# Performance work log

Measured on AMD Instinct MI355X. Metric: run time of the kernel, lower is better.

Reference implementation:

```python
import jax, jax.numpy as jnp
import numpy as np

B, S, E, H, FFN, NQ = 4, 2048, 1024, 16, 4096, 8
DK = E // H
EPS = 1e-5


def setup_inputs() -> dict:
    key = jax.random.key(0)
    ks = jax.random.split(key, 8)
    x = jax.random.normal(ks[0], (B, S, E), dtype=jnp.float32)
    theta = jax.random.normal(ks[1], (NQ,), dtype=jnp.float32)  # RY angles
    w1 = jax.random.normal(ks[2], (FFN, NQ), dtype=jnp.float32) / np.sqrt(NQ)
    b1 = jnp.zeros((FFN,), dtype=jnp.float32)
    w2 = jax.random.normal(ks[3], (E, FFN), dtype=jnp.float32) / np.sqrt(FFN)
    b2 = jnp.zeros((E,), dtype=jnp.float32)
    gamma1 = jnp.ones((E,), dtype=jnp.float32)
    beta1 = jnp.zeros((E,), dtype=jnp.float32)
    gamma2 = jnp.ones((E,), dtype=jnp.float32)
    beta2 = jnp.zeros((E,), dtype=jnp.float32)
    return {"x": x, "theta": theta, "w1": w1, "b1": b1, "w2": w2, "b2": b2,
            "gamma1": gamma1, "beta1": beta1, "gamma2": gamma2, "beta2": beta2}


def _layernorm(h, g, b):
    mu = jnp.mean(h, axis=-1, keepdims=True)
    var = jnp.mean(jnp.square(h - mu), axis=-1, keepdims=True)
    return (h - mu) * jax.lax.rsqrt(var + EPS) * g + b


def _attention(x):
    # q = k = v = separate_heads(x); no projection weights in the original.
    q = x.reshape(B, S, H, DK).transpose(0, 2, 1, 3)  # [B,H,S,DK]
    scores = jnp.einsum("bhqd,bhkd->bhqk", q, q) / np.sqrt(DK)
    probs = jax.nn.softmax(scores, axis=-1)
    out = jnp.einsum("bhqk,bhkd->bhqd", probs, q)
    return out.transpose(0, 2, 1, 3).reshape(B, S, E)


def _ffn_quantum(h, theta, w1, b1, w2, b2):
    # Per-token circuit: RX(x_i) then RY(theta_i) on independent qubits,
    # measure PauliZ -> <Z_i> = cos(x_i) * cos(theta_i). Batched over all tokens.
    qout = jnp.cos(h[..., :NQ]) * jnp.cos(theta)  # [B,S,NQ]
    hid = jax.nn.relu(jnp.einsum("bsq,fq->bsf", qout, w1) + b1)
    return jnp.einsum("bsf,ef->bse", hid, w2) + b2


def reference(x, theta, w1, b1, w2, b2, gamma1, beta1, gamma2, beta2):
    attn_out = _attention(x)
    h = _layernorm(x + attn_out, gamma1, beta1)
    ffn_out = _ffn_quantum(h, theta, w1, b1, w2, b2)
    return _layernorm(h + ffn_out, gamma2, beta2)
```

## Files before the change

kernel.cpp:

```cpp
#include <hip/hip_runtime.h>


#define Bq 4
#define Sq 2048
#define Eq 1024
#define Hq 16
#define DKq 64
#define FFNq 4096
#define NQq 8
#define LOG2E 1.44269504f

typedef unsigned int u32;
typedef unsigned short u16;
typedef _Float16 f16;
typedef f16 f16x8 __attribute__((ext_vector_type(8)));
typedef __fp16 fp16x2 __attribute__((ext_vector_type(2)));
typedef float f32x4 __attribute__((ext_vector_type(4)));
typedef float f32x16 __attribute__((ext_vector_type(16)));
typedef u32 u32x2 __attribute__((ext_vector_type(2)));
typedef u32 u32x4 __attribute__((ext_vector_type(4)));

#if __has_builtin(__builtin_amdgcn_exp2f)
#define EXP2F __builtin_amdgcn_exp2f
#else
#define EXP2F exp2f
#endif

#define MFMA(a, b, c) __builtin_amdgcn_mfma_f32_16x16x32_f16((a), (b), (c), 0, 0, 0)
#define MFMA32(a, b, c) __builtin_amdgcn_mfma_f32_32x32x16_f16((a), (b), (c), 0, 0, 0)

#define GLL(g, l)                                                          \
  __builtin_amdgcn_global_load_lds(                                        \
      (const __attribute__((address_space(1))) u32*)(g),                   \
      (__attribute__((address_space(3))) u32*)(l), 16, 0, 0)

__device__ __forceinline__ u16 f2h(float x) {
  f16 t = (f16)x;
  return __builtin_bit_cast(u16, t);
}
__device__ __forceinline__ float h2f(u16 w) {
  return (float)__builtin_bit_cast(f16, w);
}
#if __has_builtin(__builtin_amdgcn_cvt_pkrtz)
__device__ __forceinline__ u32 pkrtz(float a, float b) {
  fp16x2 r = __builtin_amdgcn_cvt_pkrtz(a, b);
  return __builtin_bit_cast(u32, r);
}
#else
__device__ __forceinline__ u32 pkrtz(float a, float b) {
  return (u32)f2h(a) | ((u32)f2h(b) << 16);
}
#endif

__device__ __forceinline__ void swap32(u32 a, u32 b, u32& r0, u32& r1) {
#if __has_builtin(__builtin_amdgcn_permlane32_swap)
  u32x2 r = __builtin_amdgcn_permlane32_swap(a, b, false, false);
  r0 = r[0];
  r1 = r[1];
#else
  u32 ax = (u32)__shfl_xor((int)a, 32);
  u32 bx = (u32)__shfl_xor((int)b, 32);
  const bool lo = (threadIdx.x & 32) == 0;
  r0 = lo ? a : bx;
  r1 = lo ? ax : b;
#endif
}

union F8 { f16x8 v; u32 w[4]; u16 h[8]; f16 e[8]; };

__global__ void k_cvt(const float* __restrict__ src, uint4* __restrict__ dst, int n8) {
  int i = blockIdx.x * 256 + threadIdx.x;
  if (i >= n8) return;
  const float4* s = (const float4*)src + 2 * (long)i;
  float4 a = s[0], b = s[1];
  uint4 r;
  r.x = pkrtz(a.x, a.y);
  r.y = pkrtz(a.z, a.w);
  r.z = pkrtz(b.x, b.y);
  r.w = pkrtz(b.z, b.w);
  dst[i] = r;
}

__global__ void k_prep(const float* __restrict__ x, u16* __restrict__ xh,
                       u16* __restrict__ xt) {
  __shared__ u16 tile[64 * 72];
  const int tid = threadIdx.x;
  const int bx = blockIdx.x;
  const int sb = bx & 31, bh = bx >> 5;
  const int b = bh >> 4, h = bh & 15;
  const int s0 = sb * 64;
  const int r = tid >> 2, cq = tid & 3;
  const float* xp = x + ((long)(b * Sq + s0 + r)) * Eq + h * 64 + cq * 16;
  float4 f0 = ((const float4*)xp)[0], f1 = ((const float4*)xp)[1];
  float4 f2 = ((const float4*)xp)[2], f3 = ((const float4*)xp)[3];
  u32 w[8];
  w[0] = pkrtz(f0.x, f0.y); w[1] = pkrtz(f0.z, f0.w);
  w[2] = pkrtz(f1.x, f1.y); w[3] = pkrtz(f1.z, f1.w);
  w[4] = pkrtz(f2.x, f2.y); w[5] = pkrtz(f2.z, f2.w);
  w[6] = pkrtz(f3.x, f3.y); w[7] = pkrtz(f3.z, f3.w);
  uint4* xo = (uint4*)(xh + ((long)(b * Sq + s0 + r)) * Eq + h * 64 + cq * 16);
  xo[0] = make_uint4(w[0], w[1], w[2], w[3]);
  xo[1] = make_uint4(w[4], w[5], w[6], w[7]);
  uint4* tp = (uint4*)(tile + r * 72 + cq * 16);
  tp[0] = make_uint4(w[0], w[1], w[2], w[3]);
  tp[1] = make_uint4(w[4], w[5], w[6], w[7]);
  __syncthreads();
  const int d = tid >> 2, rq = tid & 3;
  u32 o[8];
#pragma unroll
  for (int i = 0; i < 8; ++i) {
    u32 lo = tile[(rq * 16 + 2 * i) * 72 + d];
    u32 hi = tile[(rq * 16 + 2 * i + 1) * 72 + d];
    o[i] = lo | (hi << 16);
  }
  uint4* to = (uint4*)(xt + ((long)(bh * 64 + d)) * Sq + s0 + rq * 16);
  to[0] = make_uint4(o[0], o[1], o[2], o[3]);
  to[1] = make_uint4(o[4], o[5], o[6], o[7]);
}

__global__ __launch_bounds__(512, 4) void k_attn(const u16* __restrict__ xh,
                                                 const u16* __restrict__ xt,
                                                 u16* __restrict__ attn) {
  __shared__ __align__(16) u16 lds[16384];

  const int tid = threadIdx.x;
  const int wave = tid >> 6, lane = tid & 63;
  const int col = lane & 31;
  const int hh = lane >> 5;

  const int bx = blockIdx.x;
  const int qb = bx >> 6, bh = bx & 63;
  const int b = bh >> 4, h = bh & 15;

  const u16* xh_bh = xh + (long)b * Sq * Eq + h * 64;
  const u16* xt_bh = xt + (long)bh * 64 * Sq;

  const float SC = 0.125f * LOG2E;
  const int q = qb * 256 + wave * 32 + col;
  F8 qf[4];
  float shift;
  {
    const u16* qp = xh_bh + (long)q * Eq + hh * 8;
    float s2 = 0.f;
#pragma unroll
    for (int st = 0; st < 4; ++st) {
      F8 a;
      a.v = *(const f16x8*)(qp + st * 16);
#pragma unroll
      for (int i = 0; i < 8; ++i) {
        float v = (float)a.e[i];
        s2 += v * v;
        qf[st].e[i] = a.e[i] * (f16)SC;
      }
    }
    s2 += __shfl_xor(s2, 32);
    shift = SC * s2;
  }
  float lrow = 0.f;

  const int r8 = lane >> 3;
  const int cl = (lane & 7) ^ r8;
  const u16* gK = xh_bh + (long)(wave * 8 + r8) * Eq + cl * 8;
  const u16* gV = xt_bh + (long)(wave * 8 + r8) * Sq + cl * 8;
  const int lK = wave * 512;
  const int lV = 4096 + wave * 512;

  u16* cur = lds;
  u16* nxt = lds + 8192;

  GLL(gK, cur + lK);
  GLL(gV, cur + lV);
  gK += 64 * Eq;
  gV += 64;

  f32x16 O[2] = {};

  for (int kb = 0; kb < Sq / 64; ++kb) {
    __syncthreads();
    if (kb < Sq / 64 - 1) {
      GLL(gK, nxt + lK);
      GLL(gV, nxt + lV);
      gK += 64 * Eq;
      gV += 64;
    }
    u16* Kl = cur;
    u16* Vt = cur + 4096;

    f16x8 pf[4];
#pragma unroll
    for (int kt = 0; kt < 2; ++kt) {
      f32x16 ST;
#pragma unroll
      for (int r = 0; r < 16; ++r) ST[r] = -shift;
      const int krow = kt * 32 + col;
      const u16* kp = Kl + krow * 64;
      const int sw = krow & 7;
      __builtin_amdgcn_s_setprio(1);
#pragma unroll
      for (int st = 0; st < 4; ++st) {
        f16x8 af = *(const f16x8*)(kp + ((2 * st + hh) ^ sw) * 8);
        ST = MFMA32(af, qf[st].v, ST);
      }
      __builtin_amdgcn_s_setprio(0);

      u32 pk[8];
      float ls = 0.f;
#pragma unroll
      for (int j = 0; j < 4; ++j) {
        float p0 = EXP2F(ST[4 * j + 0]);
        float p1 = EXP2F(ST[4 * j + 1]);
        float p2 = EXP2F(ST[4 * j + 2]);
        float p3 = EXP2F(ST[4 * j + 3]);
        ls += (p0 + p1) + (p2 + p3);
        pk[2 * j] = pkrtz(p0, p1);
        pk[2 * j + 1] = pkrtz(p2, p3);
      }
      lrow += ls;
#pragma unroll
      for (int s = 0; s < 2; ++s) {
        u32 e0, e1, e2, e3;
        swap32(pk[4 * s + 0], pk[4 * s + 2], e0, e2);
        swap32(pk[4 * s + 1], pk[4 * s + 3], e1, e3);
        u32x4 wv;
        wv[0] = e0;
        wv[1] = e1;
        wv[2] = e2;
        wv[3] = e3;
        pf[kt * 2 + s] = __builtin_bit_cast(f16x8, wv);
      }
    }

    __builtin_amdgcn_s_setprio(1);
#pragma unroll
    for (int dt = 0; dt < 2; ++dt) {
      const int vrow = dt * 32 + col;
      const u16* vp = Vt + vrow * 64;
      const int sw = vrow & 7;
#pragma unroll
      for (int ks = 0; ks < 4; ++ks) {
        f16x8 vf = *(const f16x8*)(vp + ((2 * ks + hh) ^ sw) * 8);
        O[dt] = MFMA32(vf, pf[ks], O[dt]);
      }
    }
    __builtin_amdgcn_s_setprio(0);
    u16* t = cur; cur = nxt; nxt = t;
  }

  float l = lrow + __shfl_xor(lrow, 32);
  const float inv = 1.0f / l;
  u16* op = attn + (long)b * Sq * Eq + (long)q * Eq + h * 64;
#pragma unroll
  for (int dt = 0; dt < 2; ++dt) {
#pragma unroll
    for (int j = 0; j < 4; ++j) {
      const int d = dt * 32 + 8 * j + 4 * hh;
      u32 w0 = pkrtz(O[dt][4 * j + 0] * inv, O[dt][4 * j + 1] * inv);
      u32 w1 = pkrtz(O[dt][4 * j + 2] * inv, O[dt][4 * j + 3] * inv);
      *(uint2*)(op + d) = make_uint2(w0, w1);
    }
  }
}

__global__ void k_ln1(const u16* __restrict__ xh, const u16* __restrict__ attn,
                      const float* __restrict__ g, const float* __restrict__ be,
                      const float* __restrict__ theta, u16* __restrict__ hout,
                      u16* __restrict__ qout) {
  const long t = blockIdx.x;
  const int tid = threadIdx.x;
  uint2 xw = ((const uint2*)(xh + t * Eq))[tid];
  uint2 aw = ((const uint2*)(attn + t * Eq))[tid];
  float v0 = h2f(xw.x & 0xffff) + h2f(aw.x & 0xffff);
  float v1 = h2f(xw.x >> 16) + h2f(aw.x >> 16);
  float v2 = h2f(xw.y & 0xffff) + h2f(aw.y & 0xffff);
  float v3 = h2f(xw.y >> 16) + h2f(aw.y >> 16);
  float s = (v0 + v1) + (v2 + v3);
  float s2 = v0 * v0 + v1 * v1 + v2 * v2 + v3 * v3;
#pragma unroll
  for (int o = 1; o < 64; o <<= 1) {
    s += __shfl_xor(s, o);
    s2 += __shfl_xor(s2, o);
  }
  __shared__ float red[8];
  const int wv = tid >> 6, ln = tid & 63;
  if (ln == 0) { red[wv] = s; red[4 + wv] = s2; }
  __syncthreads();
  s = red[0] + red[1] + red[2] + red[3];
  s2 = red[4] + red[5] + red[6] + red[7];
  const float mu = s * (1.f / Eq);
  const float var = s2 * (1.f / Eq) - mu * mu;
  const float rstd = rsqrtf(var + 1e-5f);
  float4 gv = ((const float4*)g)[tid];
  float4 bv = ((const float4*)be)[tid];
  float o0 = (v0 - mu) * rstd * gv.x + bv.x;
  float o1 = (v1 - mu) * rstd * gv.y + bv.y;
  float o2 = (v2 - mu) * rstd * gv.z + bv.z;
  float o3 = (v3 - mu) * rstd * gv.w + bv.w;
  ((uint2*)(hout + t * Eq))[tid] = make_uint2(pkrtz(o0, o1), pkrtz(o2, o3));
  if (tid < 2) {
    float hv[4] = {o0, o1, o2, o3};
    float q[4];
#pragma unroll
    for (int i = 0; i < 4; ++i) q[i] = cosf(hv[i]) * cosf(theta[tid * 4 + i]);
    *(uint2*)(qout + t * NQq + tid * 4) = make_uint2(pkrtz(q[0], q[1]), pkrtz(q[2], q[3]));
  }
}

__global__ void k_hid(const u16* __restrict__ qout, const float* __restrict__ w1,
                      const float* __restrict__ b1, u16* __restrict__ hid) {
  __shared__ float qs[256][8];
  const int tid = threadIdx.x;
  const int fb = blockIdx.x & 63, tb = blockIdx.x >> 6;
  const int f0 = fb * 64, t0 = tb * 256;
  {
    uint4 qw = *(const uint4*)(qout + (long)(t0 + tid) * NQq);
    qs[tid][0] = h2f(qw.x & 0xffff); qs[tid][1] = h2f(qw.x >> 16);
    qs[tid][2] = h2f(qw.y & 0xffff); qs[tid][3] = h2f(qw.y >> 16);
    qs[tid][4] = h2f(qw.z & 0xffff); qs[tid][5] = h2f(qw.z >> 16);
    qs[tid][6] = h2f(qw.w & 0xffff); qs[tid][7] = h2f(qw.w >> 16);
  }
  __syncthreads();
  const int wave = tid >> 6, lane = tid & 63;
  const int f = f0 + lane;
  const float4* wp = (const float4*)(w1 + (long)f * NQq);
  float4 wa = wp[0], wb = wp[1];
  const float bb = b1[f];
  const int trow = wave * 64;
  u16* op = hid + (long)(t0 + trow) * FFNq + f;
#pragma unroll 4
  for (int i = 0; i < 64; ++i) {
    const float* q = qs[trow + i];
    float acc = bb + q[0] * wa.x + q[1] * wa.y + q[2] * wa.z + q[3] * wa.w +
                q[4] * wb.x + q[5] * wb.y + q[6] * wb.z + q[7] * wb.w;
    acc = fmaxf(acc, 0.f);
    op[(long)i * FFNq] = f2h(acc);
  }
}

__global__ __launch_bounds__(256, 2) void k_gemm(const u16* __restrict__ Ah,
                                                 const u16* __restrict__ Bh,
                                                 u16* __restrict__ C) {
  __shared__ __align__(16) u16 lds[32768];
  const int tid = threadIdx.x;
  const int wave = tid >> 6, lane = tid & 63;
  const int n = lane & 15, quad = lane >> 4;
  const int wm = wave >> 1, wn = wave & 1;
  const int m0 = (blockIdx.x >> 3) * 128;
  const int n0 = (blockIdx.x & 7) * 128;
  const int r8 = lane >> 3;
  const int cl = (lane & 7) ^ r8;

  const u16* gA[4];
  const u16* gB[4];
  int lA[4], lB[4];
#pragma unroll
  for (int j = 0; j < 4; ++j) {
    const int row = wave * 32 + j * 8;
    gA[j] = Ah + (long)(m0 + row + r8) * FFNq + cl * 8;
    gB[j] = Bh + (long)(n0 + row + r8) * FFNq + cl * 8;
    lA[j] = row * 64;
    lB[j] = 8192 + row * 64;
  }

  u16* cur = lds;
  u16* nxt = lds + 16384;

#pragma unroll
  for (int j = 0; j < 4; ++j) {
    GLL(gA[j], cur + lA[j]);
    GLL(gB[j], cur + lB[j]);
    gA[j] += 64;
    gB[j] += 64;
  }

  f32x4 acc[4][4] = {};
  for (int it = 0; it < FFNq / 64; ++it) {
    __syncthreads();
    if (it < FFNq / 64 - 1) {
#pragma unroll
      for (int j = 0; j < 4; ++j) {
        GLL(gA[j], nxt + lA[j]);
        GLL(gB[j], nxt + lB[j]);
        gA[j] += 64;
        gB[j] += 64;
      }
    }
    u16* La = cur;
    u16* Lb = cur + 8192;
#pragma unroll
    for (int c = 0; c < 2; ++c) {
      f16x8 af[4], bf[4];
#pragma unroll
      for (int i = 0; i < 4; ++i) {
        const int ra = wm * 64 + i * 16 + n;
        const int rb = wn * 64 + i * 16 + n;
        af[i] = *(const f16x8*)(La + ra * 64 + (((c * 4 + quad) ^ (n & 7)) * 8));
        bf[i] = *(const f16x8*)(Lb + rb * 64 + (((c * 4 + quad) ^ (n & 7)) * 8));
      }
#pragma unroll
      for (int i = 0; i < 4; ++i)
#pragma unroll
        for (int j = 0; j < 4; ++j) acc[i][j] = MFMA(af[i], bf[j], acc[i][j]);
    }
    u16* t = cur; cur = nxt; nxt = t;
  }
#pragma unroll
  for (int i = 0; i < 4; ++i) {
    const int row = m0 + wm * 64 + i * 16 + quad * 4;
#pragma unroll
    for (int j = 0; j < 4; ++j) {
      u16* cp = C + (long)row * Eq + n0 + wn * 64 + j * 16 + n;
      cp[0] = f2h(acc[i][j][0]);
      cp[Eq] = f2h(acc[i][j][1]);
      cp[2 * Eq] = f2h(acc[i][j][2]);
      cp[3 * Eq] = f2h(acc[i][j][3]);
    }
  }
}

__global__ void k_ln2(const u16* __restrict__ hin, const u16* __restrict__ ffn,
                      const float* __restrict__ b2, const float* __restrict__ g,
                      const float* __restrict__ be, float* __restrict__ out) {
  const long t = blockIdx.x;
  const int tid = threadIdx.x;
  uint2 hw = ((const uint2*)(hin + t * Eq))[tid];
  uint2 fw = ((const uint2*)(ffn + t * Eq))[tid];
  float4 b2v = ((const float4*)b2)[tid];
  float v0 = h2f(hw.x & 0xffff) + h2f(fw.x & 0xffff) + b2v.x;
  float v1 = h2f(hw.x >> 16) + h2f(fw.x >> 16) + b2v.y;
  float v2 = h2f(hw.y & 0xffff) + h2f(fw.y & 0xffff) + b2v.z;
  float v3 = h2f(hw.y >> 16) + h2f(fw.y >> 16) + b2v.w;
  float s = (v0 + v1) + (v2 + v3);
  float s2 = v0 * v0 + v1 * v1 + v2 * v2 + v3 * v3;
#pragma unroll
  for (int o = 1; o < 64; o <<= 1) {
    s += __shfl_xor(s, o);
    s2 += __shfl_xor(s2, o);
  }
  __shared__ float red[8];
  const int wv = tid >> 6, ln = tid & 63;
  if (ln == 0) { red[wv] = s; red[4 + wv] = s2; }
  __syncthreads();
  s = red[0] + red[1] + red[2] + red[3];
  s2 = red[4] + red[5] + red[6] + red[7];
  const float mu = s * (1.f / Eq);
  const float var = s2 * (1.f / Eq) - mu * mu;
  const float rstd = rsqrtf(var + 1e-5f);
  float4 gv = ((const float4*)g)[tid];
  float4 bv = ((const float4*)be)[tid];
  float4 o;
  o.x = (v0 - mu) * rstd * gv.x + bv.x;
  o.y = (v1 - mu) * rstd * gv.y + bv.y;
  o.z = (v2 - mu) * rstd * gv.z + bv.z;
  o.w = (v3 - mu) * rstd * gv.w + bv.w;
  ((float4*)(out + t * Eq))[tid] = o;
}

extern "C" void kernel_launch(void* const* d_in, const int* in_sizes, int n_in,
                              void* d_out, int out_size, void* d_ws, size_t ws_size,
                              hipStream_t stream) {
  const float* x = (const float*)d_in[0];
  const float* theta = (const float*)d_in[1];
  const float* w1 = (const float*)d_in[2];
  const float* b1 = (const float*)d_in[3];
  const float* w2 = (const float*)d_in[4];
  const float* b2 = (const float*)d_in[5];
  const float* g1 = (const float*)d_in[6];
  const float* be1 = (const float*)d_in[7];
  const float* g2 = (const float*)d_in[8];
  const float* be2 = (const float*)d_in[9];
  float* out = (float*)d_out;

  char* ws = (char*)d_ws;
  u16* attn = (u16*)(ws);
  u16* h = (u16*)(ws + 16777216);
  u16* xh = (u16*)(ws + 33554432);
  u16* xt = (u16*)(ws + 50331648);
  u16* ffn = (u16*)(ws + 67108864);
  u16* hid = (u16*)(ws + 83886080);
  u16* w2h = (u16*)(ws + 150994944);
  u16* qout = (u16*)(ws + 159383552);

  k_prep<<<Bq * Hq * (Sq / 64), 256, 0, stream>>>(x, xh, xt);
  k_cvt<<<2048, 256, 0, stream>>>(w2, (uint4*)w2h, (Eq * FFNq) / 8);
  k_attn<<<Bq * Hq * (Sq / 256), 512, 0, stream>>>(xh, xt, attn);
  k_ln1<<<Bq * Sq, 256, 0, stream>>>(xh, attn, g1, be1, theta, h, qout);
  k_hid<<<(Bq * Sq / 256) * (FFNq / 64), 256, 0, stream>>>(qout, w1, b1, hid);
  k_gemm<<<(Bq * Sq / 128) * (Eq / 128), 256, 0, stream>>>(hid, w2h, ffn);
  k_ln2<<<Bq * Sq, 256, 0, stream>>>(h, ffn, b2, g2, be2, out);
}
```

Measured before the change: 315.1 us.

## Process two query tiles per wave in attention to reuse K/V fragments

The attention kernel now runs 4 waves (256 threads) per block instead of 8. Each wave handles 64 query rows as two 32-row tiles, so every K and V fragment read from LDS feeds two MFMAs, halving LDS reads per FLOP. Each thread now issues two global-to-LDS loads per K/V tile instead of one. The cost is roughly double the accumulator and Q registers per thread, fewer waves to hide latency, and a lower launch-bounds occupancy hint.

```diff
diff --git a/kernel.cpp b/kernel.cpp
--- a/kernel.cpp
+++ b/kernel.cpp
@@ -118,7 +118,7 @@
   to[1] = make_uint4(o[4], o[5], o[6], o[7]);
 }
 
-__global__ __launch_bounds__(512, 4) void k_attn(const u16* __restrict__ xh,
+__global__ __launch_bounds__(256, 2) void k_attn(const u16* __restrict__ xh,
                                                  const u16* __restrict__ xt,
                                                  u16* __restrict__ attn) {
   __shared__ __align__(16) u16 lds[16384];
@@ -136,10 +136,11 @@
   const u16* xt_bh = xt + (long)bh * 64 * Sq;
 
   const float SC = 0.125f * LOG2E;
-  const int q = qb * 256 + wave * 32 + col;
-  F8 qf[4];
-  float shift;
-  {
+  F8 qf[2][4];
+  float shift[2], lrow[2] = {0.f, 0.f};
+#pragma unroll
+  for (int nt = 0; nt < 2; ++nt) {
+    const int q = qb * 256 + wave * 64 + nt * 32 + col;
     const u16* qp = xh_bh + (long)q * Eq + hh * 8;
     float s2 = 0.f;
 #pragma unroll
@@ -150,83 +151,87 @@
       for (int i = 0; i < 8; ++i) {
         float v = (float)a.e[i];
         s2 += v * v;
-        qf[st].e[i] = a.e[i] * (f16)SC;
+        qf[nt][st].e[i] = a.e[i] * (f16)SC;
       }
     }
     s2 += __shfl_xor(s2, 32);
-    shift = SC * s2;
-  }
-  float lrow = 0.f;
+    shift[nt] = SC * s2;
+  }
 
   const int r8 = lane >> 3;
   const int cl = (lane & 7) ^ r8;
-  const u16* gK = xh_bh + (long)(wave * 8 + r8) * Eq + cl * 8;
-  const u16* gV = xt_bh + (long)(wave * 8 + r8) * Sq + cl * 8;
-  const int lK = wave * 512;
-  const int lV = 4096 + wave * 512;
+  const u16* gK0 = xh_bh + (long)(wave * 16 + r8) * Eq + cl * 8;
+  const u16* gK1 = gK0 + 8 * Eq;
+  const u16* gV0 = xt_bh + (long)(wave * 16 + r8) * Sq + cl * 8;
+  const u16* gV1 = gV0 + 8 * Sq;
+  const int lK0 = wave * 1024, lK1 = lK0 + 512;
+  const int lV0 = 4096 + wave * 1024, lV1 = lV0 + 512;
 
   u16* cur = lds;
   u16* nxt = lds + 8192;
 
-  GLL(gK, cur + lK);
-  GLL(gV, cur + lV);
-  gK += 64 * Eq;
-  gV += 64;
-
-  f32x16 O[2] = {};
+  GLL(gK0, cur + lK0); GLL(gK1, cur + lK1);
+  GLL(gV0, cur + lV0); GLL(gV1, cur + lV1);
+  gK0 += 64 * Eq; gK1 += 64 * Eq; gV0 += 64; gV1 += 64;
+
+  f32x16 O[2][2] = {};
 
   for (int kb = 0; kb < Sq / 64; ++kb) {
     __syncthreads();
     if (kb < Sq / 64 - 1) {
-      GLL(gK, nxt + lK);
-      GLL(gV, nxt + lV);
-      gK += 64 * Eq;
-      gV += 64;
+      GLL(gK0, nxt + lK0); GLL(gK1, nxt + lK1);
+      GLL(gV0, nxt + lV0); GLL(gV1, nxt + lV1);
+      gK0 += 64 * Eq; gK1 += 64 * Eq; gV0 += 64; gV1 += 64;
     }
     u16* Kl = cur;
     u16* Vt = cur + 4096;
 
-    f16x8 pf[4];
+    f16x8 pf[2][4];
 #pragma unroll
     for (int kt = 0; kt < 2; ++kt) {
-      f32x16 ST;
-#pragma unroll
-      for (int r = 0; r < 16; ++r) ST[r] = -shift;
       const int krow = kt * 32 + col;
       const u16* kp = Kl + krow * 64;
       const int sw = krow & 7;
-      __builtin_amdgcn_s_setprio(1);
-#pragma unroll
-      for (int st = 0; st < 4; ++st) {
-        f16x8 af = *(const f16x8*)(kp + ((2 * st + hh) ^ sw) * 8);
-        ST = MFMA32(af, qf[st].v, ST);
-      }
-      __builtin_amdgcn_s_setprio(0);
-
-      u32 pk[8];
-      float ls = 0.f;
-#pragma unroll
-      for (int j = 0; j < 4; ++j) {
-        float p0 = EXP2F(ST[4 * j + 0]);
-        float p1 = EXP2F(ST[4 * j + 1]);
-        float p2 = EXP2F(ST[4 * j + 2]);
-        float p3 = EXP2F(ST[4 * j + 3]);
-        ls += (p0 + p1) + (p2 + p3);
-        pk[2 * j] = pkrtz(p0, p1);
-        pk[2 * j + 1] = pkrtz(p2, p3);
-      }
-      lrow += ls;
-#pragma unroll
-      for (int s = 0; s < 2; ++s) {
-        u32 e0, e1, e2, e3;
-        swap32(pk[4 * s + 0], pk[4 * s + 2], e0, e2);
-        swap32(pk[4 * s + 1], pk[4 * s + 3], e1, e3);
-        u32x4 wv;
-        wv[0] = e0;
-        wv[1] = e1;
-        wv[2] = e2;
-        wv[3] = e3;
-        pf[kt * 2 + s] = __builtin_bit_cast(f16x8, wv);
+      f16x8 af[4];
+#pragma unroll
+      for (int st = 0; st < 4; ++st)
+        af[st] = *(const f16x8*)(kp + ((2 * st + hh) ^ sw) * 8);
+
+#pragma unroll
+      for (int nt = 0; nt < 2; ++nt) {
+        f32x16 ST;
+#pragma unroll
+        for (int r = 0; r < 16; ++r) ST[r] = -shift[nt];
+        __builtin_amdgcn_s_setprio(1);
+#pragma unroll
+        for (int st = 0; st < 4; ++st) ST = MFMA32(af[st], qf[nt][st].v, ST);
+        __builtin_amdgcn_s_setprio(0);
+
+        u32 pk[8];
+        float ls = 0.f;
+#pragma unroll
+        for (int j = 0; j < 4; ++j) {
+          float p0 = EXP2F(ST[4 * j + 0]);
+          float p1 = EXP2F(ST[4 * j + 1]);
+          float p2 = EXP2F(ST[4 * j + 2]);
+          float p3 = EXP2F(ST[4 * j + 3]);
+          ls += (p0 + p1) + (p2 + p3);
+          pk[2 * j] = pkrtz(p0, p1);
+          pk[2 * j + 1] = pkrtz(p2, p3);
+        }
+        lrow[nt] += ls;
+#pragma unroll
+        for (int s = 0; s < 2; ++s) {
+          u32 e0, e1, e2, e3;
+          swap32(pk[4 * s + 0], pk[4 * s + 2], e0, e2);
+          swap32(pk[4 * s + 1], pk[4 * s + 3], e1, e3);
+          u32x4 wv;
+          wv[0] = e0;
+          wv[1] = e1;
+          wv[2] = e2;
+          wv[3] = e3;
+          pf[nt][kt * 2 + s] = __builtin_bit_cast(f16x8, wv);
+        }
       }
     }
 
@@ -239,24 +244,30 @@
 #pragma unroll
       for (int ks = 0; ks < 4; ++ks) {
         f16x8 vf = *(const f16x8*)(vp + ((2 * ks + hh) ^ sw) * 8);
-        O[dt] = MFMA32(vf, pf[ks], O[dt]);
+#pragma unroll
+        for (int nt = 0; nt < 2; ++nt)
+          O[nt][dt] = MFMA32(vf, pf[nt][ks], O[nt][dt]);
       }
     }
     __builtin_amdgcn_s_setprio(0);
     u16* t = cur; cur = nxt; nxt = t;
   }
 
-  float l = lrow + __shfl_xor(lrow, 32);
-  const float inv = 1.0f / l;
-  u16* op = attn + (long)b * Sq * Eq + (long)q * Eq + h * 64;
-#pragma unroll
-  for (int dt = 0; dt < 2; ++dt) {
-#pragma unroll
-    for (int j = 0; j < 4; ++j) {
-      const int d = dt * 32 + 8 * j + 4 * hh;
-      u32 w0 = pkrtz(O[dt][4 * j + 0] * inv, O[dt][4 * j + 1] * inv);
-      u32 w1 = pkrtz(O[dt][4 * j + 2] * inv, O[dt][4 * j + 3] * inv);
-      *(uint2*)(op + d) = make_uint2(w0, w1);
+#pragma unroll
+  for (int nt = 0; nt < 2; ++nt) {
+    float l = lrow[nt] + __shfl_xor(lrow[nt], 32);
+    const float inv = 1.0f / l;
+    const int q = qb * 256 + wave * 64 + nt * 32 + col;
+    u16* op = attn + (long)b * Sq * Eq + (long)q * Eq + h * 64;
+#pragma unroll
+    for (int dt = 0; dt < 2; ++dt) {
+#pragma unroll
+      for (int j = 0; j < 4; ++j) {
+        const int d = dt * 32 + 8 * j + 4 * hh;
+        u32 w0 = pkrtz(O[nt][dt][4 * j + 0] * inv, O[nt][dt][4 * j + 1] * inv);
+        u32 w1 = pkrtz(O[nt][dt][4 * j + 2] * inv, O[nt][dt][4 * j + 3] * inv);
+        *(uint2*)(op + d) = make_uint2(w0, w1);
+      }
     }
   }
 }
@@ -482,7 +493,7 @@
 
   k_prep<<<Bq * Hq * (Sq / 64), 256, 0, stream>>>(x, xh, xt);
   k_cvt<<<2048, 256, 0, stream>>>(w2, (uint4*)w2h, (Eq * FFNq) / 8);
-  k_attn<<<Bq * Hq * (Sq / 256), 512, 0, stream>>>(xh, xt, attn);
+  k_attn<<<Bq * Hq * (Sq / 256), 256, 0, stream>>>(xh, xt, attn);
   k_ln1<<<Bq * Sq, 256, 0, stream>>>(xh, attn, g1, be1, theta, h, qout);
   k_hid<<<(Bq * Sq / 256) * (FFNq / 64), 256, 0, stream>>>(qout, w1, b1, hid);
   k_gemm<<<(Bq * Sq / 128) * (Eq / 128), 256, 0, stream>>>(hid, w2h, ffn);
```

Result: no change. 312.4 us (-0.9%).
